# Kernel tuning notes

Measured on AMD Instinct MI355X. Metric: run time of the kernel, lower is better.

## Reference

```python
import jax, jax.numpy as jnp
import numpy as np

N = 50000
E = 800000
F_IN = 64
HID = 64


def setup_inputs() -> dict:
    key = jax.random.key(0)
    k1, k2, k3, k4, k5, k6 = jax.random.split(key, 6)
    x = jax.random.normal(k1, (N, F_IN), dtype=jnp.float32)
    edge_index = jax.random.randint(k2, (2, E), 0, N, dtype=jnp.int64)
    # GraphSAGE mean-aggregator layers: Linear(2*in -> out) applied to [x || mean_agg(x)]
    W1 = jax.random.normal(k3, (2 * F_IN, HID), dtype=jnp.float32) / np.sqrt(2 * F_IN)
    b1 = jnp.zeros((HID,), dtype=jnp.float32)
    W2 = jax.random.normal(k4, (2 * HID, HID), dtype=jnp.float32) / np.sqrt(2 * HID)
    b2 = jnp.zeros((HID,), dtype=jnp.float32)
    return {"x": x, "edge_index": edge_index, "W1": W1, "b1": b1, "W2": W2, "b2": b2}


def _sage_conv(x, src, dst, W, b):
    # mean aggregation of neighbor (src) features at dst, then linear on [self || agg]
    msg = x[src]                                                   # [E, d] gather
    s = jax.ops.segment_sum(msg, dst, num_segments=N)              # [N, d]
    cnt = jax.ops.segment_sum(jnp.ones((src.shape[0], 1), x.dtype), dst, num_segments=N)
    agg = s / jnp.maximum(cnt, 1.0)
    return jnp.concatenate([x, agg], axis=-1) @ W + b


def reference(x, edge_index, W1, b1, W2, b2):
    src, dst = edge_index[0], edge_index[1]
    h = _sage_conv(x, src, dst, W1, b1)
    h = jax.nn.relu(h)  # dropout is identity at inference
    h = _sage_conv(h, src, dst, W2, b2)
    return h
```

## Files before the change

### kernel.cpp

```cpp
#include <hip/hip_runtime.h>

#define N_NODES 50000
#define N_EDGES 800000
#define F 64
#define CHUNK 3072
#define NWG1 ((N_EDGES + CHUNK - 1) / CHUNK)
#define NBUCK 196
#define BSTRIDE 8192
#define NWTILE (N_NODES / 16)
#define NSENT N_NODES

typedef __attribute__((ext_vector_type(8))) _Float16 half8;
typedef __attribute__((ext_vector_type(4))) float f32x4;
typedef __attribute__((ext_vector_type(8))) unsigned short ushort8v;

__global__ __launch_bounds__(256) void partition_conv(
    const int*    __restrict__ src, const int* __restrict__ dst,
    const float4* __restrict__ xin,
    half8*        __restrict__ x16,
    unsigned short* __restrict__ h116,
    const float*  __restrict__ W1, const float* __restrict__ W2,
    _Float16*     __restrict__ Wt1, _Float16* __restrict__ Wt2,
    unsigned*     __restrict__ bcur,
    unsigned*     __restrict__ ebuf) {
  int t = threadIdx.x, b = blockIdx.x;
  if (b == NWG1) {
    for (int i = t; i < 64 * 128; i += 256) {
      int n = i >> 7, k = i & 127;
      Wt1[i] = (_Float16)W1[k * 64 + n];
      Wt2[i] = (_Float16)W2[k * 64 + n];
    }
    if (t < 32) ((unsigned*)(x16 + (size_t)NSENT * 8))[t] = 0;
    if (t >= 64 && t < 96) ((unsigned*)h116)[(size_t)NSENT * 32 + (t - 64)] = 0;
    return;
  }
  __shared__ int hist[256], lscan[256], lcur[256], gbase[256];
  __shared__ unsigned stage[CHUNK];
  hist[t] = 0; __syncthreads();
  int e0 = b * CHUNK;
  int cnt = N_EDGES - e0; if (cnt > CHUNK) cnt = CHUNK;
  for (int i = t; i < cnt; i += 256) atomicAdd(&hist[dst[e0 + i] >> 8], 1);

  const int TOT = N_NODES * F / 8;
  for (int i = b * 256 + t; i < TOT; i += NWG1 * 256) {
    float4 a = xin[i * 2], c = xin[i * 2 + 1];
    half8 hh;
    hh[0] = (_Float16)a.x; hh[1] = (_Float16)a.y;
    hh[2] = (_Float16)a.z; hh[3] = (_Float16)a.w;
    hh[4] = (_Float16)c.x; hh[5] = (_Float16)c.y;
    hh[6] = (_Float16)c.z; hh[7] = (_Float16)c.w;
    x16[i] = hh;
  }
  __syncthreads();

  int v = hist[t];
  lscan[t] = v; __syncthreads();
  for (int off = 1; off < 256; off <<= 1) {
    int a = (t >= off) ? lscan[t - off] : 0;
    __syncthreads();
    lscan[t] += a;
    __syncthreads();
  }
  lscan[t] -= v;
  lcur[t] = lscan[t];
  if (v > 0) gbase[t] = (int)atomicAdd(&bcur[t], (unsigned)v);
  __syncthreads();

  for (int i = t; i < cnt; i += 256) {
    int d = dst[e0 + i], s = src[e0 + i];
    int bb = d >> 8;
    int p = atomicAdd(&lcur[bb], 1);
    stage[p] = ((unsigned)bb << 24) | ((unsigned)(d & 255) << 16) | (unsigned)s;
  }
  __syncthreads();
  for (int i = t; i < cnt; i += 256) {
    unsigned e = stage[i];
    int bb = e >> 24;
    ebuf[bb * BSTRIDE + gbase[bb] + (i - lscan[bb])] = e;
  }
}

__global__ __launch_bounds__(256) void bucket_sort(
    const unsigned* __restrict__ ebuf, const unsigned* __restrict__ bcur,
    unsigned short* __restrict__ edge_src, int* __restrict__ row_start,
    int* __restrict__ deg, unsigned char* __restrict__ perm) {
  __shared__ int lhist[128], lscan[128], lcur[128];
  __shared__ unsigned short srt[BSTRIDE / 2];
  int B = blockIdx.x, t = threadIdx.x;
  int b = B >> 1, h = B & 1;
  int s0 = b * BSTRIDE;
  int cnt = (int)bcur[b];

  if (t < 128) lhist[t] = 0;
  __syncthreads();
  for (int i = t; i < cnt; i += 256) {
    int bin = (int)((ebuf[s0 + i] >> 16) & 255);
    if ((bin >> 7) == h) atomicAdd(&lhist[bin & 127], 1);
  }
  __syncthreads();

  int v  = (t < 128) ? lhist[t] : 0;
  int pv = (v + 7) & ~7;
  if (t < 128) lscan[t] = pv;
  __syncthreads();
  for (int off = 1; off < 128; off <<= 1) {
    int a = (t >= off && t < 128) ? lscan[t - off] : 0;
    __syncthreads();
    if (t < 128) lscan[t] += a;
    __syncthreads();
  }
  if (t < 128) { lscan[t] -= pv; lcur[t] = lscan[t]; }
  __syncthreads();

  int total_p = lscan[127] + ((lhist[127] + 7) & ~7);
  int base    = h * (BSTRIDE / 2);

  for (int i = t; i < cnt; i += 256) {
    unsigned e = ebuf[s0 + i];
    int bin = (int)((e >> 16) & 255);
    if ((bin >> 7) == h) {
      int p = atomicAdd(&lcur[bin & 127], 1);
      srt[p] = (unsigned short)(e & 0xFFFFu);
    }
  }
  __syncthreads();
  if (t < 128) {
    int p0 = lscan[t];
    for (int j = v; j < pv; ++j) srt[p0 + j] = (unsigned short)NSENT;
  }
  __syncthreads();

  for (int i = t; i < total_p; i += 256) edge_src[s0 + base + i] = srt[i];

  if (t < 128) {
    int n = b * 256 + h * 128 + t;
    if (n < N_NODES) { row_start[n] = s0 + base + lscan[t]; deg[n] = v; }
    int g0 = t & ~31;
    int rank = 0;
    #pragma unroll 8
    for (int j = 0; j < 32; ++j) {
      int dj = lhist[g0 + j];
      rank += (dj < v) || (dj == v && j < (t & 31));
    }
    perm[b * 256 + h * 128 + g0 + rank] = (unsigned char)(t & 31);
  }
}

__global__ __launch_bounds__(256) void sage_layer_fused(
    const half8*    __restrict__ feat16,
    const _Float16* __restrict__ self16,
    const int*      __restrict__ row_start,
    const int*      __restrict__ deg,
    const unsigned short* __restrict__ edge_src,
    const unsigned char* __restrict__ perm,
    const _Float16* __restrict__ Wt,
    const float*    __restrict__ bias,
    float*          __restrict__ outf,
    unsigned short* __restrict__ out16,
    int do_relu) {
  __shared__ _Float16 lmean[32 * 72];
  int t = threadIdx.x;
  int w = t >> 6, lane = t & 63;

  {
    int o = lane >> 3, q = lane & 7;
    int ln = (int)perm[blockIdx.x * 32 + w * 8 + o];
    int n = blockIdx.x * 32 + ln;
    if (n < N_NODES) {
      int start = row_start[n];
      int d     = deg[n];
      half8 acc8 = (half8){0, 0, 0, 0, 0, 0, 0, 0};
      if (d > 0) {
        const ushort8v* idp = (const ushort8v*)(edge_src + start);
        int nb = (d + 7) >> 3;
        ushort8v iv = idp[0];
        for (int b = 0; b < nb; ++b) {
          half8 h0 = feat16[(size_t)iv[0] * 8 + q];
          half8 h1 = feat16[(size_t)iv[1] * 8 + q];
          half8 h2 = feat16[(size_t)iv[2] * 8 + q];
          half8 h3 = feat16[(size_t)iv[3] * 8 + q];
          half8 h4 = feat16[(size_t)iv[4] * 8 + q];
          half8 h5 = feat16[(size_t)iv[5] * 8 + q];
          half8 h6 = feat16[(size_t)iv[6] * 8 + q];
          half8 h7 = feat16[(size_t)iv[7] * 8 + q];
          ushort8v nv;
          bool more = (b + 1 < nb);
          if (more) nv = idp[b + 1];
          acc8 += h0; acc8 += h1; acc8 += h2; acc8 += h3;
          acc8 += h4; acc8 += h5; acc8 += h6; acc8 += h7;
          if (more) iv = nv;
        }
      }
      float inv = (d > 0) ? 1.0f / (float)d : 0.0f;
      half8 hm;
      #pragma unroll
      for (int k = 0; k < 8; ++k) hm[k] = (_Float16)((float)acc8[k] * inv);
      *(half8*)&lmean[ln * 72 + q * 8] = hm;
    }
  }
  __syncthreads();

  int tile = w >> 1;
  int wt = blockIdx.x * 2 + tile;
  if (wt >= NWTILE) return;
  int m = lane & 15, quad = lane >> 4;
  size_t arow = (size_t)(wt * 16 + m) * 64 + quad * 8;
  half8 a0 = *(const half8*)(self16 + arow);
  half8 a1 = *(const half8*)(self16 + arow + 32);
  int ln = tile * 16 + m;
  half8 a2 = *(const half8*)&lmean[ln * 72 + quad * 8];
  half8 a3 = *(const half8*)&lmean[ln * 72 + quad * 8 + 32];

  int nt0 = (w & 1) * 2;
  #pragma unroll
  for (int i = 0; i < 2; ++i) {
    int nt = nt0 + i;
    float bv = bias[nt * 16 + m];
    f32x4 acc = (f32x4){bv, bv, bv, bv};
    const _Float16* wrow = Wt + (size_t)(nt * 16 + m) * 128 + quad * 8;
    half8 b0 = *(const half8*)(wrow);
    half8 b1 = *(const half8*)(wrow + 32);
    half8 b2 = *(const half8*)(wrow + 64);
    half8 b3 = *(const half8*)(wrow + 96);
    acc = __builtin_amdgcn_mfma_f32_16x16x32_f16(a0, b0, acc, 0, 0, 0);
    acc = __builtin_amdgcn_mfma_f32_16x16x32_f16(a1, b1, acc, 0, 0, 0);
    acc = __builtin_amdgcn_mfma_f32_16x16x32_f16(a2, b2, acc, 0, 0, 0);
    acc = __builtin_amdgcn_mfma_f32_16x16x32_f16(a3, b3, acc, 0, 0, 0);
    #pragma unroll
    for (int r = 0; r < 4; ++r) {
      size_t off = (size_t)(wt * 16 + quad * 4 + r) * 64 + nt * 16 + m;
      float v = acc[r];
      if (do_relu) v = fmaxf(v, 0.0f);
      if (outf)  outf[off] = v;
      if (out16) { _Float16 hv = (_Float16)v; out16[off] = *(unsigned short*)&hv; }
    }
  }
}

extern "C" void kernel_launch(void* const* d_in, const int* in_sizes, int n_in,
                              void* d_out, int out_size, void* d_ws, size_t ws_size,
                              hipStream_t stream) {
  const float* x  = (const float*)d_in[0];
  const int*   ei = (const int*)d_in[1];
  const float* W1 = (const float*)d_in[2];
  const float* b1 = (const float*)d_in[3];
  const float* W2 = (const float*)d_in[4];
  const float* b2 = (const float*)d_in[5];
  float* out = (float*)d_out;

  const int* src = ei;
  const int* dst = ei + N_EDGES;

  int* wsi       = (int*)d_ws;
  unsigned* bcur = (unsigned*)wsi;
  int* deg       = wsi + 256;
  int* row_start = wsi + 50304;
  unsigned short* edge_src = (unsigned short*)(wsi + 100352);
  unsigned* ebuf = (unsigned*)(wsi + 903168);
  half8* x16     = (half8*)(wsi + 2508800);
  unsigned short* h116 = (unsigned short*)(wsi + 4109312);
  _Float16* Wt1  = (_Float16*)(wsi + 5709824);
  _Float16* Wt2  = (_Float16*)(wsi + 5713920);
  unsigned char* perm = (unsigned char*)(wsi + 5718016);

  hipMemsetAsync(bcur, 0, 256 * sizeof(unsigned), stream);

  dim3 blk(256);
  partition_conv<<<NWG1 + 1, blk, 0, stream>>>(
      src, dst, (const float4*)x, x16, h116, W1, W2, Wt1, Wt2, bcur, ebuf);
  bucket_sort<<<NBUCK * 2, blk, 0, stream>>>(ebuf, bcur, edge_src, row_start,
                                             deg, perm);

  dim3 grd_fused((N_NODES + 31) / 32);

  sage_layer_fused<<<grd_fused, blk, 0, stream>>>(
      x16, (const _Float16*)x16, row_start, deg, edge_src, perm,
      Wt1, b1, nullptr, h116, 1);
  sage_layer_fused<<<grd_fused, blk, 0, stream>>>(
      (const half8*)h116, (const _Float16*)h116, row_start, deg, edge_src, perm,
      Wt2, b2, out, nullptr, 0);
}
```

Baseline: 144.8 us.

## Split each node's neighbor list by source-index half to improve gather locality

The bucket sort now bins edges by destination and by whether the source index is below or above the midpoint. Each half is padded separately to a multiple of 8, and both half-degrees are packed into the deg array. The fused layer runs two gather loops per node, low-half sources first and then high-half sources, so concurrent wavefronts touch a narrower feature range and should get better cache locality. In exchange it adds sentinel padding, meaning more wasted loads per node, plus a longer 256-entry scan and extra loop overhead.

```diff
diff --git a/kernel.cpp b/kernel.cpp
--- a/kernel.cpp
+++ b/kernel.cpp
@@ -9,6 +9,7 @@
 #define BSTRIDE 8192
 #define NWTILE (N_NODES / 16)
 #define NSENT N_NODES
+#define SRCMID 25000
 
 typedef __attribute__((ext_vector_type(8))) _Float16 half8;
 typedef __attribute__((ext_vector_type(4))) float f32x4;
@@ -84,47 +85,53 @@
     const unsigned* __restrict__ ebuf, const unsigned* __restrict__ bcur,
     unsigned short* __restrict__ edge_src, int* __restrict__ row_start,
     int* __restrict__ deg, unsigned char* __restrict__ perm) {
-  __shared__ int lhist[128], lscan[128], lcur[128];
+  __shared__ int lhist[256], lscan[256], lcur[256];
   __shared__ unsigned short srt[BSTRIDE / 2];
   int B = blockIdx.x, t = threadIdx.x;
   int b = B >> 1, h = B & 1;
   int s0 = b * BSTRIDE;
   int cnt = (int)bcur[b];
 
-  if (t < 128) lhist[t] = 0;
-  __syncthreads();
-  for (int i = t; i < cnt; i += 256) {
-    int bin = (int)((ebuf[s0 + i] >> 16) & 255);
-    if ((bin >> 7) == h) atomicAdd(&lhist[bin & 127], 1);
-  }
-  __syncthreads();
-
-  int v  = (t < 128) ? lhist[t] : 0;
-  int pv = (v + 7) & ~7;
-  if (t < 128) lscan[t] = pv;
-  __syncthreads();
-  for (int off = 1; off < 128; off <<= 1) {
-    int a = (t >= off && t < 128) ? lscan[t - off] : 0;
-    __syncthreads();
-    if (t < 128) lscan[t] += a;
-    __syncthreads();
-  }
-  if (t < 128) { lscan[t] -= pv; lcur[t] = lscan[t]; }
-  __syncthreads();
-
-  int total_p = lscan[127] + ((lhist[127] + 7) & ~7);
-  int base    = h * (BSTRIDE / 2);
-
+  lhist[t] = 0;
+  __syncthreads();
   for (int i = t; i < cnt; i += 256) {
     unsigned e = ebuf[s0 + i];
-    int bin = (int)((e >> 16) & 255);
-    if ((bin >> 7) == h) {
-      int p = atomicAdd(&lcur[bin & 127], 1);
+    int obin = (int)((e >> 16) & 255);
+    if ((obin >> 7) == h) {
+      int bin = ((obin & 127) << 1) | ((e & 0xFFFFu) >= (unsigned)SRCMID);
+      atomicAdd(&lhist[bin], 1);
+    }
+  }
+  __syncthreads();
+
+  int v  = lhist[t];
+  int pv = (v + 7) & ~7;
+  lscan[t] = pv;
+  __syncthreads();
+  for (int off = 1; off < 256; off <<= 1) {
+    int a = (t >= off) ? lscan[t - off] : 0;
+    __syncthreads();
+    lscan[t] += a;
+    __syncthreads();
+  }
+  lscan[t] -= pv;
+  lcur[t] = lscan[t];
+  __syncthreads();
+
+  int total_p = lscan[255] + ((lhist[255] + 7) & ~7);
+  int base    = h * (BSTRIDE / 2);
+
+  for (int i = t; i < cnt; i += 256) {
+    unsigned e = ebuf[s0 + i];
+    int obin = (int)((e >> 16) & 255);
+    if ((obin >> 7) == h) {
+      int bin = ((obin & 127) << 1) | ((e & 0xFFFFu) >= (unsigned)SRCMID);
+      int p = atomicAdd(&lcur[bin], 1);
       srt[p] = (unsigned short)(e & 0xFFFFu);
     }
   }
   __syncthreads();
-  if (t < 128) {
+  {
     int p0 = lscan[t];
     for (int j = v; j < pv; ++j) srt[p0 + j] = (unsigned short)NSENT;
   }
@@ -134,17 +141,44 @@
 
   if (t < 128) {
     int n = b * 256 + h * 128 + t;
-    if (n < N_NODES) { row_start[n] = s0 + base + lscan[t]; deg[n] = v; }
-    int g0 = t & ~31;
+    int vlo = lhist[2 * t], vhi = lhist[2 * t + 1];
+    if (n < N_NODES) {
+      row_start[n] = s0 + base + lscan[2 * t];
+      deg[n] = vlo | (vhi << 16);
+    }
+    int g0 = t & ~31, me = t & 31, vt = vlo + vhi;
     int rank = 0;
     #pragma unroll 8
     for (int j = 0; j < 32; ++j) {
-      int dj = lhist[g0 + j];
-      rank += (dj < v) || (dj == v && j < (t & 31));
-    }
-    perm[b * 256 + h * 128 + g0 + rank] = (unsigned char)(t & 31);
+      int dj = lhist[2 * (g0 + j)] + lhist[2 * (g0 + j) + 1];
+      rank += (dj < vt) || (dj == vt && j < me);
+    }
+    perm[b * 256 + h * 128 + g0 + rank] = (unsigned char)me;
   }
 }
+
+#define GATHER_LOOP(IDP, NB)                                        \
+  {                                                                 \
+    const ushort8v* idp_ = (IDP);                                   \
+    int nb_ = (NB);                                                 \
+    ushort8v iv = idp_[0];                                          \
+    for (int b_ = 0; b_ < nb_; ++b_) {                              \
+      half8 h0 = feat16[(size_t)iv[0] * 8 + q];                     \
+      half8 h1 = feat16[(size_t)iv[1] * 8 + q];                     \
+      half8 h2 = feat16[(size_t)iv[2] * 8 + q];                     \
+      half8 h3 = feat16[(size_t)iv[3] * 8 + q];                     \
+      half8 h4 = feat16[(size_t)iv[4] * 8 + q];                     \
+      half8 h5 = feat16[(size_t)iv[5] * 8 + q];                     \
+      half8 h6 = feat16[(size_t)iv[6] * 8 + q];                     \
+      half8 h7 = feat16[(size_t)iv[7] * 8 + q];                     \
+      ushort8v nv;                                                  \
+      bool more = (b_ + 1 < nb_);                                   \
+      if (more) nv = idp_[b_ + 1];                                  \
+      acc8 += h0; acc8 += h1; acc8 += h2; acc8 += h3;               \
+      acc8 += h4; acc8 += h5; acc8 += h6; acc8 += h7;               \
+      if (more) iv = nv;                                            \
+    }                                                               \
+  }
 
 __global__ __launch_bounds__(256) void sage_layer_fused(
     const half8*    __restrict__ feat16,
@@ -168,29 +202,13 @@
     int n = blockIdx.x * 32 + ln;
     if (n < N_NODES) {
       int start = row_start[n];
-      int d     = deg[n];
+      int dpack = deg[n];
+      int dl = dpack & 0xFFFF, dh = dpack >> 16;
+      int d  = dl + dh;
       half8 acc8 = (half8){0, 0, 0, 0, 0, 0, 0, 0};
-      if (d > 0) {
-        const ushort8v* idp = (const ushort8v*)(edge_src + start);
-        int nb = (d + 7) >> 3;
-        ushort8v iv = idp[0];
-        for (int b = 0; b < nb; ++b) {
-          half8 h0 = feat16[(size_t)iv[0] * 8 + q];
-          half8 h1 = feat16[(size_t)iv[1] * 8 + q];
-          half8 h2 = feat16[(size_t)iv[2] * 8 + q];
-          half8 h3 = feat16[(size_t)iv[3] * 8 + q];
-          half8 h4 = feat16[(size_t)iv[4] * 8 + q];
-          half8 h5 = feat16[(size_t)iv[5] * 8 + q];
-          half8 h6 = feat16[(size_t)iv[6] * 8 + q];
-          half8 h7 = feat16[(size_t)iv[7] * 8 + q];
-          ushort8v nv;
-          bool more = (b + 1 < nb);
-          if (more) nv = idp[b + 1];
-          acc8 += h0; acc8 += h1; acc8 += h2; acc8 += h3;
-          acc8 += h4; acc8 += h5; acc8 += h6; acc8 += h7;
-          if (more) iv = nv;
-        }
-      }
+      if (dl > 0) GATHER_LOOP((const ushort8v*)(edge_src + start), (dl + 7) >> 3);
+      if (dh > 0) GATHER_LOOP((const ushort8v*)(edge_src + start + ((dl + 7) & ~7)),
+                              (dh + 7) >> 3);
       float inv = (d > 0) ? 1.0f / (float)d : 0.0f;
       half8 hm;
       #pragma unroll
```

Result: no change. 147.0 us (+1.5%).

## Replace global atomic bucket offsets with fixed-capacity per-block slots

Applied to the files above, without the earlier changes.

The partition kernel now writes each block's per-bucket edge count into a count matrix and stores edges in fixed slots of 48 per (bucket, block) pair. This removes the global atomicAdd on bucket cursors and the memset launch that cleared them. The bucket-sort kernel walks all slots, skipping empty ones by checking the stored counts. In exchange, bucket_sort reads a sparser, larger slot grid with integer division. Any (bucket, block) pair holding more than 48 edges silently drops the extras, so correctness depends on destination indices being roughly uniform.

```diff
diff --git a/kernel.cpp b/kernel.cpp
--- a/kernel.cpp
+++ b/kernel.cpp
@@ -7,6 +7,7 @@
 #define NWG1 ((N_EDGES + CHUNK - 1) / CHUNK)
 #define NBUCK 196
 #define BSTRIDE 8192
+#define CAP 48
 #define NWTILE (N_NODES / 16)
 #define NSENT N_NODES
 
@@ -21,8 +22,8 @@
     unsigned short* __restrict__ h116,
     const float*  __restrict__ W1, const float* __restrict__ W2,
     _Float16*     __restrict__ Wt1, _Float16* __restrict__ Wt2,
-    unsigned*     __restrict__ bcur,
-    unsigned*     __restrict__ ebuf) {
+    int*          __restrict__ cntbuf,
+    unsigned*     __restrict__ ebuf2) {
   int t = threadIdx.x, b = blockIdx.x;
   if (b == NWG1) {
     for (int i = t; i < 64 * 128; i += 256) {
@@ -34,7 +35,7 @@
     if (t >= 64 && t < 96) ((unsigned*)h116)[(size_t)NSENT * 32 + (t - 64)] = 0;
     return;
   }
-  __shared__ int hist[256], lscan[256], lcur[256], gbase[256];
+  __shared__ int hist[256], lscan[256], lcur[256];
   __shared__ unsigned stage[CHUNK];
   hist[t] = 0; __syncthreads();
   int e0 = b * CHUNK;
@@ -54,6 +55,7 @@
   __syncthreads();
 
   int v = hist[t];
+  if (t < NBUCK) cntbuf[t * NWG1 + b] = v;
   lscan[t] = v; __syncthreads();
   for (int off = 1; off < 256; off <<= 1) {
     int a = (t >= off) ? lscan[t - off] : 0;
@@ -63,7 +65,6 @@
   }
   lscan[t] -= v;
   lcur[t] = lscan[t];
-  if (v > 0) gbase[t] = (int)atomicAdd(&bcur[t], (unsigned)v);
   __syncthreads();
 
   for (int i = t; i < cnt; i += 256) {
@@ -76,26 +77,34 @@
   for (int i = t; i < cnt; i += 256) {
     unsigned e = stage[i];
     int bb = e >> 24;
-    ebuf[bb * BSTRIDE + gbase[bb] + (i - lscan[bb])] = e;
+    int pos = i - lscan[bb];
+    if (pos < CAP)
+      ebuf2[(size_t)(bb * NWG1 + b) * CAP + pos] = e;
   }
 }
 
 __global__ __launch_bounds__(256) void bucket_sort(
-    const unsigned* __restrict__ ebuf, const unsigned* __restrict__ bcur,
+    const int* __restrict__ cntbuf, const unsigned* __restrict__ ebuf2,
     unsigned short* __restrict__ edge_src, int* __restrict__ row_start,
     int* __restrict__ deg, unsigned char* __restrict__ perm) {
   __shared__ int lhist[128], lscan[128], lcur[128];
+  __shared__ int kcnt[NWG1];
   __shared__ unsigned short srt[BSTRIDE / 2];
   int B = blockIdx.x, t = threadIdx.x;
   int b = B >> 1, h = B & 1;
-  int s0 = b * BSTRIDE;
-  int cnt = (int)bcur[b];
 
   if (t < 128) lhist[t] = 0;
-  __syncthreads();
-  for (int i = t; i < cnt; i += 256) {
-    int bin = (int)((ebuf[s0 + i] >> 16) & 255);
-    if ((bin >> 7) == h) atomicAdd(&lhist[bin & 127], 1);
+  for (int k = t; k < NWG1; k += 256) kcnt[k] = cntbuf[b * NWG1 + k];
+  __syncthreads();
+
+  const int TOTSLOT = NWG1 * CAP;
+  for (int i = t; i < TOTSLOT; i += 256) {
+    int k = i / CAP, j = i - k * CAP;
+    if (j < kcnt[k]) {
+      unsigned e = ebuf2[(size_t)(b * NWG1 + k) * CAP + j];
+      int obin = (int)((e >> 16) & 255);
+      if ((obin >> 7) == h) atomicAdd(&lhist[obin & 127], 1);
+    }
   }
   __syncthreads();
 
@@ -114,13 +123,17 @@
 
   int total_p = lscan[127] + ((lhist[127] + 7) & ~7);
   int base    = h * (BSTRIDE / 2);
-
-  for (int i = t; i < cnt; i += 256) {
-    unsigned e = ebuf[s0 + i];
-    int bin = (int)((e >> 16) & 255);
-    if ((bin >> 7) == h) {
-      int p = atomicAdd(&lcur[bin & 127], 1);
-      srt[p] = (unsigned short)(e & 0xFFFFu);
+  int s0      = b * BSTRIDE;
+
+  for (int i = t; i < TOTSLOT; i += 256) {
+    int k = i / CAP, j = i - k * CAP;
+    if (j < kcnt[k]) {
+      unsigned e = ebuf2[(size_t)(b * NWG1 + k) * CAP + j];
+      int obin = (int)((e >> 16) & 255);
+      if ((obin >> 7) == h) {
+        int p = atomicAdd(&lcur[obin & 127], 1);
+        srt[p] = (unsigned short)(e & 0xFFFFu);
+      }
     }
   }
   __syncthreads();
@@ -252,23 +265,21 @@
   const int* dst = ei + N_EDGES;
 
   int* wsi       = (int*)d_ws;
-  unsigned* bcur = (unsigned*)wsi;
-  int* deg       = wsi + 256;
-  int* row_start = wsi + 50304;
-  unsigned short* edge_src = (unsigned short*)(wsi + 100352);
-  unsigned* ebuf = (unsigned*)(wsi + 903168);
-  half8* x16     = (half8*)(wsi + 2508800);
-  unsigned short* h116 = (unsigned short*)(wsi + 4109312);
-  _Float16* Wt1  = (_Float16*)(wsi + 5709824);
-  _Float16* Wt2  = (_Float16*)(wsi + 5713920);
-  unsigned char* perm = (unsigned char*)(wsi + 5718016);
-
-  hipMemsetAsync(bcur, 0, 256 * sizeof(unsigned), stream);
+  int* cntbuf    = wsi;
+  int* deg       = wsi + 51200;
+  int* row_start = wsi + 101248;
+  unsigned short* edge_src = (unsigned short*)(wsi + 151296);
+  unsigned* ebuf2 = (unsigned*)(wsi + 954112);
+  half8* x16     = (half8*)(wsi + 3409664);
+  unsigned short* h116 = (unsigned short*)(wsi + 5010176);
+  _Float16* Wt1  = (_Float16*)(wsi + 6610688);
+  _Float16* Wt2  = (_Float16*)(wsi + 6614784);
+  unsigned char* perm = (unsigned char*)(wsi + 6618880);
 
   dim3 blk(256);
   partition_conv<<<NWG1 + 1, blk, 0, stream>>>(
-      src, dst, (const float4*)x, x16, h116, W1, W2, Wt1, Wt2, bcur, ebuf);
-  bucket_sort<<<NBUCK * 2, blk, 0, stream>>>(ebuf, bcur, edge_src, row_start,
+      src, dst, (const float4*)x, x16, h116, W1, W2, Wt1, Wt2, cntbuf, ebuf2);
+  bucket_sort<<<NBUCK * 2, blk, 0, stream>>>(cntbuf, ebuf2, edge_src, row_start,
                                              deg, perm);
 
   dim3 grd_fused((N_NODES + 31) / 32);
```

Measured after the change: 165.5 us. 1.14x slower.
